# Performance work log

Hardware: AMD Instinct MI355X
Metric: run time of the kernel (lower is better)

## Reference

```python
import jax, jax.numpy as jnp
import numpy as np

H, KV, HD = 32, 4, 64
REP = H // KV
MAX_POS = 2048


def setup_inputs() -> dict:
    key = jax.random.key(0)
    ks = jax.random.split(key, 6)
    B, S, D = 2, 1024, 2048
    x = jax.random.normal(ks[0], (B, S, D), dtype=jnp.float32)
    wq = jax.random.normal(ks[1], (D, H * HD), dtype=jnp.float32) * 0.02
    wk = jax.random.normal(ks[2], (D, KV * HD), dtype=jnp.float32) * 0.02
    wv = jax.random.normal(ks[3], (D, KV * HD), dtype=jnp.float32) * 0.02
    wo = jax.random.normal(ks[4], (H * HD, D), dtype=jnp.float32) * 0.02
    # RoPE tables: [max_pos, head_dim//2]
    inv_freq = 1.0 / (10000.0 ** (np.arange(0, HD, 2, dtype=np.float32) / HD))
    angles = np.arange(MAX_POS, dtype=np.float32)[:, None] * inv_freq[None, :]
    cos = jnp.asarray(np.cos(angles), dtype=jnp.float32)
    sin = jnp.asarray(np.sin(angles), dtype=jnp.float32)
    # causal additive mask [S, S]
    row = jnp.arange(S)[:, None]
    col = jnp.arange(S)[None, :]
    mask = jnp.where(col <= row, 0.0, -1e9).astype(jnp.float32)
    return {"x": x, "wq": wq, "wk": wk, "wv": wv, "wo": wo,
            "cos": cos, "sin": sin, "mask": mask, "pos": 0}


def _rotate(t, c, s):
    # t: [B,S,Hx,HD]; c,s: [1,S,1,HD//2]
    half = t.shape[-1] // 2
    t1, t2 = t[..., :half], t[..., half:]
    return jnp.concatenate([t1 * c - t2 * s, t2 * c + t1 * s], axis=-1)


def reference(x, wq, wk, wv, wo, cos, sin, mask, pos):
    B, S, D = x.shape
    q = (x @ wq).reshape(B, S, H, HD)
    k = (x @ wk).reshape(B, S, KV, HD)
    v = (x @ wv).reshape(B, S, KV, HD)
    c = cos[pos:pos + S][None, :, None, :]
    s = sin[pos:pos + S][None, :, None, :]
    q = _rotate(q, c, s)
    k = _rotate(k, c, s)
    # prefill: cache[:, 0:S] == fresh k,v, kv_len == S
    # native GQA broadcast: group q heads by kv head instead of repeating k/v
    qg = q.reshape(B, S, KV, REP, HD)
    scores = jnp.einsum('bqkrd,bskd->bkrqs', qg, k) / jnp.sqrt(jnp.float32(HD))
    scores = scores + mask  # mask broadcasts over [B,KV,REP,S,S]
    attn = jax.nn.softmax(scores, axis=-1)
    out = jnp.einsum('bkrqs,bskd->bqkrd', attn, v).reshape(B, S, H * HD)
    return out @ wo
```

## Files before the change

### kernel.cpp

```cpp
#include <hip/hip_runtime.h>

#define B_ 2
#define S_ 1024
#define D_ 2048
#define H_ 32
#define KV_ 4
#define HD_ 64
#define NQKV 2560

typedef __attribute__((ext_vector_type(8))) short bf16x8;
typedef __attribute__((ext_vector_type(4))) float f32x4;

__device__ __forceinline__ unsigned short f2bf(float f) {
  unsigned int u = __float_as_uint(f);
  u = (u + 0x7fffu + ((u >> 16) & 1u)) >> 16;
  return (unsigned short)u;
}

__global__ __launch_bounds__(256) void k_convert(const float* __restrict__ src,
                                                 unsigned short* __restrict__ dst, int n4) {
  int i = blockIdx.x * 256 + threadIdx.x;
  if (i >= n4) return;
  float4 v = ((const float4*)src)[i];
  ushort4 o;
  o.x = f2bf(v.x); o.y = f2bf(v.y); o.z = f2bf(v.z); o.w = f2bf(v.w);
  ((ushort4*)dst)[i] = o;
}

__global__ __launch_bounds__(256) void k_transpose(const float* __restrict__ src,
                                                   unsigned short* __restrict__ dst,
                                                   int K, int N, int roff, int dld) {
  __shared__ float tile[32][33];
  int n0 = blockIdx.x * 32, k0 = blockIdx.y * 32;
  int tx = threadIdx.x & 31, ty = threadIdx.x >> 5;
  #pragma unroll
  for (int i = 0; i < 4; ++i)
    tile[ty + 8 * i][tx] = src[(size_t)(k0 + ty + 8 * i) * N + (n0 + tx)];
  __syncthreads();
  #pragma unroll
  for (int i = 0; i < 4; ++i)
    dst[(size_t)(roff + n0 + ty + 8 * i) * dld + (k0 + tx)] = f2bf(tile[tx][ty + 8 * i]);
}

template <int BM, int BN, int MODE>
__global__ __launch_bounds__(256) void k_gemm(const unsigned short* __restrict__ A,
                                              const unsigned short* __restrict__ Bt,
                                              float* __restrict__ C,
                                              const float* __restrict__ cosT,
                                              const float* __restrict__ sinT,
                                              const int* __restrict__ posp,
                                              unsigned short* __restrict__ q_r,
                                              unsigned short* __restrict__ k_r,
                                              unsigned short* __restrict__ v_t,
                                              int M, int N, int K) {
  constexpr int MR = BM / 32;
  constexpr int NR = BN / 32;
  __shared__ alignas(16) unsigned short As[BM * 64];
  __shared__ alignas(16) unsigned short Bs[BN * 64];
  const int tid = threadIdx.x;
  const int wid = tid >> 6, lane = tid & 63;
  const int lo = lane & 15, hi = lane >> 4;
  const int m0 = blockIdx.y * BM, n0 = blockIdx.x * BN;
  const int wr = wid >> 1, wc = wid & 1;
  f32x4 acc[MR][NR] = {};

  const int nkt = K >> 6;
  for (int kt = 0; kt < nkt; ++kt) {
    __syncthreads();
    #pragma unroll
    for (int u = tid; u < BM * 8; u += 256) {
      int row = u >> 3, ch = u & 7, chs = ch ^ (row & 7);
      const unsigned short* ga = A + (size_t)(m0 + row) * K + kt * 64 + chs * 8;
      __builtin_amdgcn_global_load_lds((const __attribute__((address_space(1))) void*)ga,
                                       (__attribute__((address_space(3))) void*)(As + u * 8), 16, 0, 0);
    }
    #pragma unroll
    for (int u = tid; u < BN * 8; u += 256) {
      int row = u >> 3, ch = u & 7, chs = ch ^ (row & 7);
      const unsigned short* gb = Bt + (size_t)(n0 + row) * K + kt * 64 + chs * 8;
      __builtin_amdgcn_global_load_lds((const __attribute__((address_space(1))) void*)gb,
                                       (__attribute__((address_space(3))) void*)(Bs + u * 8), 16, 0, 0);
    }
    __syncthreads();
    #pragma unroll
    for (int ks = 0; ks < 2; ++ks) {
      const int chs = (ks * 4 + hi) ^ (lo & 7);
      bf16x8 a[MR], b[NR];
      #pragma unroll
      for (int m = 0; m < MR; ++m) {
        int row = wr * (BM / 2) + m * 16 + lo;
        a[m] = *(const bf16x8*)(As + row * 64 + chs * 8);
      }
      #pragma unroll
      for (int n = 0; n < NR; ++n) {
        int row = wc * (BN / 2) + n * 16 + lo;
        b[n] = *(const bf16x8*)(Bs + row * 64 + chs * 8);
      }
      #pragma unroll
      for (int m = 0; m < MR; ++m)
        #pragma unroll
        for (int n = 0; n < NR; ++n)
          acc[m][n] = __builtin_amdgcn_mfma_f32_16x16x32_bf16(a[m], b[n], acc[m][n], 0, 0, 0);
    }
  }

  if (MODE == 0) {
    const int cr = hi * 4;
    #pragma unroll
    for (int m = 0; m < MR; ++m)
      #pragma unroll
      for (int n = 0; n < NR; ++n) {
        int col = n0 + wc * (BN / 2) + n * 16 + lo;
        int rowb = m0 + wr * (BM / 2) + m * 16 + cr;
        #pragma unroll
        for (int r = 0; r < 4; ++r)
          C[(size_t)(rowb + r) * N + col] = acc[m][n][r];
      }
  } else {
    const int col0 = n0 + wc * (BN / 2);
    const int pos = posp[0];
    if (col0 < 2048) {
      const int h = col0 >> 6;
      #pragma unroll
      for (int m = 0; m < MR; ++m)
        #pragma unroll
        for (int r = 0; r < 4; ++r) {
          int row = m0 + wr * (BM / 2) + m * 16 + hi * 4 + r;
          int s = row & (S_ - 1), b = row >> 10;
          unsigned short* base = q_r + ((size_t)(b * H_ + h) * S_ + s) * HD_;
          #pragma unroll
          for (int np = 0; np < 2; ++np) {
            int i = np * 16 + lo;
            float t1 = acc[m][np][r], t2 = acc[m][np + 2][r];
            float c = cosT[(size_t)(pos + s) * 32 + i];
            float sn = sinT[(size_t)(pos + s) * 32 + i];
            base[i] = f2bf(t1 * c - t2 * sn);
            base[i + 32] = f2bf(t2 * c + t1 * sn);
          }
        }
    } else if (col0 < 2304) {
      const int g = (col0 - 2048) >> 6;
      #pragma unroll
      for (int m = 0; m < MR; ++m)
        #pragma unroll
        for (int r = 0; r < 4; ++r) {
          int row = m0 + wr * (BM / 2) + m * 16 + hi * 4 + r;
          int s = row & (S_ - 1), b = row >> 10;
          unsigned short* base = k_r + ((size_t)(b * KV_ + g) * S_ + s) * HD_;
          #pragma unroll
          for (int np = 0; np < 2; ++np) {
            int i = np * 16 + lo;
            float t1 = acc[m][np][r], t2 = acc[m][np + 2][r];
            float c = cosT[(size_t)(pos + s) * 32 + i];
            float sn = sinT[(size_t)(pos + s) * 32 + i];
            base[i] = f2bf(t1 * c - t2 * sn);
            base[i + 32] = f2bf(t2 * c + t1 * sn);
          }
        }
    } else {
      const int g = (col0 - 2304) >> 6;
      #pragma unroll
      for (int m = 0; m < MR; ++m) {
        int row0 = m0 + wr * (BM / 2) + m * 16 + hi * 4;
        int s0 = row0 & (S_ - 1), b = row0 >> 10;
        #pragma unroll
        for (int n = 0; n < NR; ++n) {
          int d = n * 16 + lo;
          ushort4 o;
          o.x = f2bf(acc[m][n][0]);
          o.y = f2bf(acc[m][n][1]);
          o.z = f2bf(acc[m][n][2]);
          o.w = f2bf(acc[m][n][3]);
          *(ushort4*)(v_t + ((size_t)(b * KV_ + g) * HD_ + d) * S_ + s0) = o;
        }
      }
    }
  }
}

__global__ __launch_bounds__(256) void k_attn(const unsigned short* __restrict__ qr,
                                              const unsigned short* __restrict__ kr,
                                              const unsigned short* __restrict__ vt,
                                              unsigned short* __restrict__ ao) {
  __shared__ alignas(16) unsigned short k_lds[64 * 64];
  __shared__ alignas(16) unsigned short v_lds[64 * 64];
  const int tid = threadIdx.x;
  const int wid = tid >> 6, lane = tid & 63;
  const int lo = lane & 15, hi = lane >> 4;
  const int b = blockIdx.z, h = blockIdx.y, g = h >> 3;
  const int qt = blockIdx.x;
  const int qb = qt * 64 + wid * 16;
  const int q = qb + lo;

  const unsigned short* qrow = qr + ((size_t)(b * H_ + h) * S_ + q) * HD_;
  bf16x8 qf[2];
  qf[0] = *(const bf16x8*)(qrow + hi * 8);
  qf[1] = *(const bf16x8*)(qrow + 32 + hi * 8);

  const unsigned short* kbase = kr + (size_t)(b * KV_ + g) * S_ * HD_;
  const unsigned short* vbase = vt + (size_t)(b * KV_ + g) * HD_ * S_;

  f32x4 oacc[4] = {};
  float mrun = -1e30f, lrun = 0.f;
  const float kscale = 0.125f;

  for (int c = 0; c <= qt; ++c) {
    const int j0 = c * 64;
    __syncthreads();
    #pragma unroll
    for (int i = 0; i < 2; ++i) {
      int u = i * 256 + tid;
      int r = u >> 3, ch = u & 7;
      int chs = ch ^ (r & 7);
      const unsigned short* gk = kbase + (size_t)(j0 + r) * HD_ + chs * 8;
      __builtin_amdgcn_global_load_lds((const __attribute__((address_space(1))) void*)gk,
                                       (__attribute__((address_space(3))) void*)(k_lds + u * 8), 16, 0, 0);
      const unsigned short* gv = vbase + (size_t)r * S_ + j0 + chs * 8;
      __builtin_amdgcn_global_load_lds((const __attribute__((address_space(1))) void*)gv,
                                       (__attribute__((address_space(3))) void*)(v_lds + u * 8), 16, 0, 0);
    }
    __syncthreads();

    f32x4 st[4];
    #pragma unroll
    for (int jt = 0; jt < 4; ++jt) st[jt] = (f32x4){0.f, 0.f, 0.f, 0.f};
    #pragma unroll
    for (int ks = 0; ks < 2; ++ks)
      #pragma unroll
      for (int jt = 0; jt < 4; ++jt) {
        int row = jt * 16 + lo;
        int chs = (ks * 4 + hi) ^ (lo & 7);
        bf16x8 kf = *(const bf16x8*)(k_lds + row * 64 + chs * 8);
        st[jt] = __builtin_amdgcn_mfma_f32_16x16x32_bf16(kf, qf[ks], st[jt], 0, 0, 0);
      }

    const bool diag = (c == qt);
    float pmax = -1e30f;
    #pragma unroll
    for (int jt = 0; jt < 4; ++jt)
      #pragma unroll
      for (int rr = 0; rr < 4; ++rr) {
        float sc = st[jt][rr] * kscale;
        if (diag && (j0 + jt * 16 + hi * 4 + rr > q)) sc = -1e30f;
        st[jt][rr] = sc;
        pmax = fmaxf(pmax, sc);
      }
    pmax = fmaxf(pmax, __shfl_xor(pmax, 16, 64));
    pmax = fmaxf(pmax, __shfl_xor(pmax, 32, 64));
    float mn = fmaxf(mrun, pmax);
    float scale = __expf(mrun - mn);
    float ps = 0.f;
    #pragma unroll
    for (int jt = 0; jt < 4; ++jt)
      #pragma unroll
      for (int rr = 0; rr < 4; ++rr) {
        float e = __expf(st[jt][rr] - mn);
        st[jt][rr] = e;
        ps += e;
      }
    ps += __shfl_xor(ps, 16, 64);
    ps += __shfl_xor(ps, 32, 64);
    lrun = lrun * scale + ps;
    mrun = mn;
    #pragma unroll
    for (int dt = 0; dt < 4; ++dt)
      #pragma unroll
      for (int rr = 0; rr < 4; ++rr) oacc[dt][rr] *= scale;

    unsigned int pk[4][2];
    #pragma unroll
    for (int jt = 0; jt < 4; ++jt)
      #pragma unroll
      for (int cp = 0; cp < 2; ++cp)
        pk[jt][cp] = (unsigned int)f2bf(st[jt][2 * cp]) |
                     ((unsigned int)f2bf(st[jt][2 * cp + 1]) << 16);

    int s0l = ((hi & 1) << 5) + lo;
    int s1l = s0l + 16;
    bool hb = (hi & 2) != 0;
    bf16x8 pf[2];
    #pragma unroll
    for (int ks = 0; ks < 2; ++ks) {
      unsigned int a0 = __shfl((int)pk[2 * ks][0], s0l, 64);
      unsigned int b0 = __shfl((int)pk[2 * ks + 1][0], s0l, 64);
      unsigned int a1 = __shfl((int)pk[2 * ks][1], s0l, 64);
      unsigned int b1 = __shfl((int)pk[2 * ks + 1][1], s0l, 64);
      unsigned int a2 = __shfl((int)pk[2 * ks][0], s1l, 64);
      unsigned int b2 = __shfl((int)pk[2 * ks + 1][0], s1l, 64);
      unsigned int a3 = __shfl((int)pk[2 * ks][1], s1l, 64);
      unsigned int b3 = __shfl((int)pk[2 * ks + 1][1], s1l, 64);
      union { unsigned int u[4]; bf16x8 v; } cvt;
      cvt.u[0] = hb ? b0 : a0;
      cvt.u[1] = hb ? b1 : a1;
      cvt.u[2] = hb ? b2 : a2;
      cvt.u[3] = hb ? b3 : a3;
      pf[ks] = cvt.v;
    }

    #pragma unroll
    for (int ks = 0; ks < 2; ++ks)
      #pragma unroll
      for (int dt = 0; dt < 4; ++dt) {
        int row = dt * 16 + lo;
        int chs = (ks * 4 + hi) ^ (lo & 7);
        bf16x8 vf = *(const bf16x8*)(v_lds + row * 64 + chs * 8);
        oacc[dt] = __builtin_amdgcn_mfma_f32_16x16x32_bf16(vf, pf[ks], oacc[dt], 0, 0, 0);
      }
  }

  float inv = 1.f / lrun;
  #pragma unroll
  for (int dt = 0; dt < 4; ++dt) {
    ushort4 o;
    o.x = f2bf(oacc[dt][0] * inv);
    o.y = f2bf(oacc[dt][1] * inv);
    o.z = f2bf(oacc[dt][2] * inv);
    o.w = f2bf(oacc[dt][3] * inv);
    *(ushort4*)(ao + ((size_t)(b * S_ + q)) * (H_ * HD_) + h * HD_ + dt * 16 + hi * 4) = o;
  }
}

extern "C" void kernel_launch(void* const* d_in, const int* in_sizes, int n_in,
                              void* d_out, int out_size, void* d_ws, size_t ws_size,
                              hipStream_t stream) {
  const float* x    = (const float*)d_in[0];
  const float* wq   = (const float*)d_in[1];
  const float* wk   = (const float*)d_in[2];
  const float* wv   = (const float*)d_in[3];
  const float* wo   = (const float*)d_in[4];
  const float* cosT = (const float*)d_in[5];
  const float* sinT = (const float*)d_in[6];
  const int*   posp = (const int*)d_in[8];
  float* out = (float*)d_out;

  char* ws = (char*)d_ws;
  size_t off = 0;
  auto alloc = [&](size_t bytes) {
    char* p = ws + off;
    off += (bytes + 255) & ~(size_t)255;
    return p;
  };
  unsigned short* xb  = (unsigned short*)alloc((size_t)B_ * S_ * D_ * 2);
  unsigned short* wft = (unsigned short*)alloc((size_t)NQKV * D_ * 2);
  unsigned short* wot = (unsigned short*)alloc((size_t)D_ * D_ * 2);
  unsigned short* q_r = (unsigned short*)alloc((size_t)B_ * H_ * S_ * HD_ * 2);
  unsigned short* k_r = (unsigned short*)alloc((size_t)B_ * KV_ * S_ * HD_ * 2);
  unsigned short* v_t = (unsigned short*)alloc((size_t)B_ * KV_ * HD_ * S_ * 2);
  unsigned short* ao  = (unsigned short*)alloc((size_t)B_ * S_ * H_ * HD_ * 2);
  if (off > ws_size) return;

  k_convert<<<(B_ * S_ * D_ / 4 + 255) / 256, 256, 0, stream>>>(x, xb, B_ * S_ * D_ / 4);
  k_transpose<<<dim3(D_ / 32, D_ / 32), 256, 0, stream>>>(wq, wft, D_, D_, 0, D_);
  k_transpose<<<dim3((KV_ * HD_) / 32, D_ / 32), 256, 0, stream>>>(wk, wft, D_, KV_ * HD_, 2048, D_);
  k_transpose<<<dim3((KV_ * HD_) / 32, D_ / 32), 256, 0, stream>>>(wv, wft, D_, KV_ * HD_, 2304, D_);
  k_transpose<<<dim3(D_ / 32, D_ / 32), 256, 0, stream>>>(wo, wot, D_, D_, 0, D_);

  k_gemm<64, 128, 1><<<dim3(NQKV / 128, (B_ * S_) / 64), 256, 0, stream>>>(
      xb, wft, nullptr, cosT, sinT, posp, q_r, k_r, v_t, B_ * S_, NQKV, D_);

  k_attn<<<dim3(S_ / 64, H_, B_), 256, 0, stream>>>(q_r, k_r, v_t, ao);

  k_gemm<64, 128, 0><<<dim3(D_ / 128, (B_ * S_) / 64), 256, 0, stream>>>(
      ao, wot, out, nullptr, nullptr, nullptr, nullptr, nullptr, nullptr, B_ * S_, D_, D_);
}
```

Baseline: 127.3 us.

## Double-buffer K/V tiles and pair causal query tiles per attention block

The attention kernel now double-buffers the K/V LDS tiles, prefetching the next chunk while computing the current one, so one barrier per iteration replaces two. Each block processes two query tiles (qt and its mirror from the end) so every block does equal causal work, halving the grid. MFMA sections are wrapped in s_setprio to favour matrix work. This doubles LDS use and halves the block count, which may reduce occupancy and parallelism across CUs.

```diff
diff --git a/kernel.cpp b/kernel.cpp
--- a/kernel.cpp
+++ b/kernel.cpp
@@ -182,31 +182,20 @@
                                               const unsigned short* __restrict__ kr,
                                               const unsigned short* __restrict__ vt,
                                               unsigned short* __restrict__ ao) {
-  __shared__ alignas(16) unsigned short k_lds[64 * 64];
-  __shared__ alignas(16) unsigned short v_lds[64 * 64];
+  __shared__ alignas(16) unsigned short k_lds[2][64 * 64];
+  __shared__ alignas(16) unsigned short v_lds[2][64 * 64];
   const int tid = threadIdx.x;
   const int wid = tid >> 6, lane = tid & 63;
   const int lo = lane & 15, hi = lane >> 4;
   const int b = blockIdx.z, h = blockIdx.y, g = h >> 3;
-  const int qt = blockIdx.x;
-  const int qb = qt * 64 + wid * 16;
-  const int q = qb + lo;
-
-  const unsigned short* qrow = qr + ((size_t)(b * H_ + h) * S_ + q) * HD_;
-  bf16x8 qf[2];
-  qf[0] = *(const bf16x8*)(qrow + hi * 8);
-  qf[1] = *(const bf16x8*)(qrow + 32 + hi * 8);
+  const float kscale = 0.125f;
 
   const unsigned short* kbase = kr + (size_t)(b * KV_ + g) * S_ * HD_;
   const unsigned short* vbase = vt + (size_t)(b * KV_ + g) * HD_ * S_;
-
-  f32x4 oacc[4] = {};
-  float mrun = -1e30f, lrun = 0.f;
-  const float kscale = 0.125f;
-
-  for (int c = 0; c <= qt; ++c) {
+  int buf = 0;
+
+  auto stage = [&](int c, int bi) {
     const int j0 = c * 64;
-    __syncthreads();
     #pragma unroll
     for (int i = 0; i < 2; ++i) {
       int u = i * 256 + tid;
@@ -214,110 +203,140 @@
       int chs = ch ^ (r & 7);
       const unsigned short* gk = kbase + (size_t)(j0 + r) * HD_ + chs * 8;
       __builtin_amdgcn_global_load_lds((const __attribute__((address_space(1))) void*)gk,
-                                       (__attribute__((address_space(3))) void*)(k_lds + u * 8), 16, 0, 0);
+                                       (__attribute__((address_space(3))) void*)(k_lds[bi] + u * 8), 16, 0, 0);
       const unsigned short* gv = vbase + (size_t)r * S_ + j0 + chs * 8;
       __builtin_amdgcn_global_load_lds((const __attribute__((address_space(1))) void*)gv,
-                                       (__attribute__((address_space(3))) void*)(v_lds + u * 8), 16, 0, 0);
-    }
+                                       (__attribute__((address_space(3))) void*)(v_lds[bi] + u * 8), 16, 0, 0);
+    }
+  };
+
+  auto processTile = [&](int qt) {
+    const int q = qt * 64 + wid * 16 + lo;
+    const unsigned short* qrow = qr + ((size_t)(b * H_ + h) * S_ + q) * HD_;
+    bf16x8 qf[2];
+    qf[0] = *(const bf16x8*)(qrow + hi * 8);
+    qf[1] = *(const bf16x8*)(qrow + 32 + hi * 8);
+
+    f32x4 oacc[4] = {};
+    float mrun = -1e30f, lrun = 0.f;
+
+    stage(0, buf);
     __syncthreads();
 
-    f32x4 st[4];
-    #pragma unroll
-    for (int jt = 0; jt < 4; ++jt) st[jt] = (f32x4){0.f, 0.f, 0.f, 0.f};
-    #pragma unroll
-    for (int ks = 0; ks < 2; ++ks)
-      #pragma unroll
-      for (int jt = 0; jt < 4; ++jt) {
-        int row = jt * 16 + lo;
-        int chs = (ks * 4 + hi) ^ (lo & 7);
-        bf16x8 kf = *(const bf16x8*)(k_lds + row * 64 + chs * 8);
-        st[jt] = __builtin_amdgcn_mfma_f32_16x16x32_bf16(kf, qf[ks], st[jt], 0, 0, 0);
-      }
-
-    const bool diag = (c == qt);
-    float pmax = -1e30f;
-    #pragma unroll
-    for (int jt = 0; jt < 4; ++jt)
-      #pragma unroll
-      for (int rr = 0; rr < 4; ++rr) {
-        float sc = st[jt][rr] * kscale;
-        if (diag && (j0 + jt * 16 + hi * 4 + rr > q)) sc = -1e30f;
-        st[jt][rr] = sc;
-        pmax = fmaxf(pmax, sc);
-      }
-    pmax = fmaxf(pmax, __shfl_xor(pmax, 16, 64));
-    pmax = fmaxf(pmax, __shfl_xor(pmax, 32, 64));
-    float mn = fmaxf(mrun, pmax);
-    float scale = __expf(mrun - mn);
-    float ps = 0.f;
-    #pragma unroll
-    for (int jt = 0; jt < 4; ++jt)
-      #pragma unroll
-      for (int rr = 0; rr < 4; ++rr) {
-        float e = __expf(st[jt][rr] - mn);
-        st[jt][rr] = e;
-        ps += e;
-      }
-    ps += __shfl_xor(ps, 16, 64);
-    ps += __shfl_xor(ps, 32, 64);
-    lrun = lrun * scale + ps;
-    mrun = mn;
-    #pragma unroll
-    for (int dt = 0; dt < 4; ++dt)
-      #pragma unroll
-      for (int rr = 0; rr < 4; ++rr) oacc[dt][rr] *= scale;
-
-    unsigned int pk[4][2];
-    #pragma unroll
-    for (int jt = 0; jt < 4; ++jt)
-      #pragma unroll
-      for (int cp = 0; cp < 2; ++cp)
-        pk[jt][cp] = (unsigned int)f2bf(st[jt][2 * cp]) |
-                     ((unsigned int)f2bf(st[jt][2 * cp + 1]) << 16);
-
-    int s0l = ((hi & 1) << 5) + lo;
-    int s1l = s0l + 16;
-    bool hb = (hi & 2) != 0;
-    bf16x8 pf[2];
-    #pragma unroll
-    for (int ks = 0; ks < 2; ++ks) {
-      unsigned int a0 = __shfl((int)pk[2 * ks][0], s0l, 64);
-      unsigned int b0 = __shfl((int)pk[2 * ks + 1][0], s0l, 64);
-      unsigned int a1 = __shfl((int)pk[2 * ks][1], s0l, 64);
-      unsigned int b1 = __shfl((int)pk[2 * ks + 1][1], s0l, 64);
-      unsigned int a2 = __shfl((int)pk[2 * ks][0], s1l, 64);
-      unsigned int b2 = __shfl((int)pk[2 * ks + 1][0], s1l, 64);
-      unsigned int a3 = __shfl((int)pk[2 * ks][1], s1l, 64);
-      unsigned int b3 = __shfl((int)pk[2 * ks + 1][1], s1l, 64);
-      union { unsigned int u[4]; bf16x8 v; } cvt;
-      cvt.u[0] = hb ? b0 : a0;
-      cvt.u[1] = hb ? b1 : a1;
-      cvt.u[2] = hb ? b2 : a2;
-      cvt.u[3] = hb ? b3 : a3;
-      pf[ks] = cvt.v;
-    }
-
-    #pragma unroll
-    for (int ks = 0; ks < 2; ++ks)
-      #pragma unroll
-      for (int dt = 0; dt < 4; ++dt) {
-        int row = dt * 16 + lo;
-        int chs = (ks * 4 + hi) ^ (lo & 7);
-        bf16x8 vf = *(const bf16x8*)(v_lds + row * 64 + chs * 8);
-        oacc[dt] = __builtin_amdgcn_mfma_f32_16x16x32_bf16(vf, pf[ks], oacc[dt], 0, 0, 0);
-      }
-  }
-
-  float inv = 1.f / lrun;
-  #pragma unroll
-  for (int dt = 0; dt < 4; ++dt) {
-    ushort4 o;
-    o.x = f2bf(oacc[dt][0] * inv);
-    o.y = f2bf(oacc[dt][1] * inv);
-    o.z = f2bf(oacc[dt][2] * inv);
-    o.w = f2bf(oacc[dt][3] * inv);
-    *(ushort4*)(ao + ((size_t)(b * S_ + q)) * (H_ * HD_) + h * HD_ + dt * 16 + hi * 4) = o;
-  }
+    for (int c = 0; c <= qt; ++c) {
+      if (c < qt) stage(c + 1, buf ^ 1);
+      const int j0 = c * 64;
+      const unsigned short* kl = k_lds[buf];
+      const unsigned short* vl = v_lds[buf];
+
+      f32x4 st[4];
+      #pragma unroll
+      for (int jt = 0; jt < 4; ++jt) st[jt] = (f32x4){0.f, 0.f, 0.f, 0.f};
+      __builtin_amdgcn_s_setprio(1);
+      #pragma unroll
+      for (int ks = 0; ks < 2; ++ks)
+        #pragma unroll
+        for (int jt = 0; jt < 4; ++jt) {
+          int row = jt * 16 + lo;
+          int chs = (ks * 4 + hi) ^ (lo & 7);
+          bf16x8 kf = *(const bf16x8*)(kl + row * 64 + chs * 8);
+          st[jt] = __builtin_amdgcn_mfma_f32_16x16x32_bf16(kf, qf[ks], st[jt], 0, 0, 0);
+        }
+      __builtin_amdgcn_s_setprio(0);
+
+      const bool diag = (c == qt);
+      float pmax = -1e30f;
+      #pragma unroll
+      for (int jt = 0; jt < 4; ++jt)
+        #pragma unroll
+        for (int rr = 0; rr < 4; ++rr) {
+          float sc = st[jt][rr] * kscale;
+          if (diag && (j0 + jt * 16 + hi * 4 + rr > q)) sc = -1e30f;
+          st[jt][rr] = sc;
+          pmax = fmaxf(pmax, sc);
+        }
+      pmax = fmaxf(pmax, __shfl_xor(pmax, 16, 64));
+      pmax = fmaxf(pmax, __shfl_xor(pmax, 32, 64));
+      float mn = fmaxf(mrun, pmax);
+      float scale = __expf(mrun - mn);
+      float ps = 0.f;
+      #pragma unroll
+      for (int jt = 0; jt < 4; ++jt)
+        #pragma unroll
+        for (int rr = 0; rr < 4; ++rr) {
+          float e = __expf(st[jt][rr] - mn);
+          st[jt][rr] = e;
+          ps += e;
+        }
+      ps += __shfl_xor(ps, 16, 64);
+      ps += __shfl_xor(ps, 32, 64);
+      lrun = lrun * scale + ps;
+      mrun = mn;
+      #pragma unroll
+      for (int dt = 0; dt < 4; ++dt)
+        #pragma unroll
+        for (int rr = 0; rr < 4; ++rr) oacc[dt][rr] *= scale;
+
+      unsigned int pk[4][2];
+      #pragma unroll
+      for (int jt = 0; jt < 4; ++jt)
+        #pragma unroll
+        for (int cp = 0; cp < 2; ++cp)
+          pk[jt][cp] = (unsigned int)f2bf(st[jt][2 * cp]) |
+                       ((unsigned int)f2bf(st[jt][2 * cp + 1]) << 16);
+
+      int s0l = ((hi & 1) << 5) + lo;
+      int s1l = s0l + 16;
+      bool hb = (hi & 2) != 0;
+      bf16x8 pf[2];
+      #pragma unroll
+      for (int ks = 0; ks < 2; ++ks) {
+        unsigned int a0 = __shfl((int)pk[2 * ks][0], s0l, 64);
+        unsigned int b0 = __shfl((int)pk[2 * ks + 1][0], s0l, 64);
+        unsigned int a1 = __shfl((int)pk[2 * ks][1], s0l, 64);
+        unsigned int b1 = __shfl((int)pk[2 * ks + 1][1], s0l, 64);
+        unsigned int a2 = __shfl((int)pk[2 * ks][0], s1l, 64);
+        unsigned int b2 = __shfl((int)pk[2 * ks + 1][0], s1l, 64);
+        unsigned int a3 = __shfl((int)pk[2 * ks][1], s1l, 64);
+        unsigned int b3 = __shfl((int)pk[2 * ks + 1][1], s1l, 64);
+        union { unsigned int u[4]; bf16x8 v; } cvt;
+        cvt.u[0] = hb ? b0 : a0;
+        cvt.u[1] = hb ? b1 : a1;
+        cvt.u[2] = hb ? b2 : a2;
+        cvt.u[3] = hb ? b3 : a3;
+        pf[ks] = cvt.v;
+      }
+
+      __builtin_amdgcn_s_setprio(1);
+      #pragma unroll
+      for (int ks = 0; ks < 2; ++ks)
+        #pragma unroll
+        for (int dt = 0; dt < 4; ++dt) {
+          int row = dt * 16 + lo;
+          int chs = (ks * 4 + hi) ^ (lo & 7);
+          bf16x8 vf = *(const bf16x8*)(vl + row * 64 + chs * 8);
+          oacc[dt] = __builtin_amdgcn_mfma_f32_16x16x32_bf16(vf, pf[ks], oacc[dt], 0, 0, 0);
+        }
+      __builtin_amdgcn_s_setprio(0);
+
+      __syncthreads();
+      if (c < qt) buf ^= 1;
+    }
+
+    float inv = 1.f / lrun;
+    #pragma unroll
+    for (int dt = 0; dt < 4; ++dt) {
+      ushort4 o;
+      o.x = f2bf(oacc[dt][0] * inv);
+      o.y = f2bf(oacc[dt][1] * inv);
+      o.z = f2bf(oacc[dt][2] * inv);
+      o.w = f2bf(oacc[dt][3] * inv);
+      *(ushort4*)(ao + ((size_t)(b * S_ + q)) * (H_ * HD_) + h * HD_ + dt * 16 + hi * 4) = o;
+    }
+  };
+
+  processTile(blockIdx.x);
+  processTile((S_ / 64 - 1) - blockIdx.x);
 }
 
 extern "C" void kernel_launch(void* const* d_in, const int* in_sizes, int n_in,
@@ -358,7 +377,7 @@
   k_gemm<64, 128, 1><<<dim3(NQKV / 128, (B_ * S_) / 64), 256, 0, stream>>>(
       xb, wft, nullptr, cosT, sinT, posp, q_r, k_r, v_t, B_ * S_, NQKV, D_);
 
-  k_attn<<<dim3(S_ / 64, H_, B_), 256, 0, stream>>>(q_r, k_r, v_t, ao);
+  k_attn<<<dim3(S_ / 128, H_, B_), 256, 0, stream>>>(q_r, k_r, v_t, ao);
 
   k_gemm<64, 128, 0><<<dim3(D_ / 128, (B_ * S_) / 64), 256, 0, stream>>>(
       ao, wot, out, nullptr, nullptr, nullptr, nullptr, nullptr, nullptr, B_ * S_, D_, D_);
```

After: 116.7 us. 1.09x faster.
